# Kernel tuning notes

Hardware: AMD Instinct MI355X
Metric: run time of the kernel (lower is better)

## Reference

```python
import jax, jax.numpy as jnp
import numpy as np

N = 50000
E = 800000
R = 8
F_IN = 128
H = 128


def setup_inputs() -> dict:
    key = jax.random.key(0)
    ks = jax.random.split(key, 16)
    x = jax.random.normal(ks[0], (N, F_IN), dtype=jnp.float32)
    edge_index = jax.random.randint(ks[1], (2, E), 0, N, dtype=jnp.int64)
    edge_type = jax.random.randint(ks[2], (E,), 0, R, dtype=jnp.int64)
    s = 0.05
    params = {
        'W1': jax.random.normal(ks[3], (R, F_IN, H), jnp.float32) * s,
        'root1': jax.random.normal(ks[4], (F_IN, H), jnp.float32) * s,
        'b1': jnp.zeros((H,), jnp.float32),
        'W2': jax.random.normal(ks[5], (R, H, H), jnp.float32) * s,
        'root2': jax.random.normal(ks[6], (H, H), jnp.float32) * s,
        'b2': jnp.zeros((H,), jnp.float32),
        'W3': jax.random.normal(ks[7], (R, H, H), jnp.float32) * s,
        'root3': jax.random.normal(ks[8], (H, H), jnp.float32) * s,
        'b3': jnp.zeros((H,), jnp.float32),
        'fc_w': jax.random.normal(ks[9], (H, 1), jnp.float32) * s,
        'fc_b': jnp.zeros((1,), jnp.float32),
    }
    return dict(x=x, edge_index=edge_index, edge_type=edge_type, **params)


def _rgcn_conv(x, W, Wroot, b, src, dst, etype):
    # PyG RGCNConv with mean aggregation per (dst, relation):
    # out_i = x_i @ Wroot + b + sum_r mean_{j in N_r(i)} (x_j @ W_r)
    xw = jnp.einsum('nf,rfh->rnh', x, W)          # [R, N, H] per-relation transform
    m = xw[etype, src]                             # [E, H] gathered messages
    seg = dst * R + etype                          # composite (dst, rel) segment id
    deg = jax.ops.segment_sum(jnp.ones((m.shape[0],), x.dtype), seg, num_segments=N * R)
    norm = jnp.where(deg > 0, 1.0 / deg, 0.0)[seg]  # [E]
    agg = jax.ops.segment_sum(m * norm[:, None], dst, num_segments=N)  # [N, H]
    return agg + x @ Wroot + b


def reference(x, edge_index, edge_type, W1, root1, b1, W2, root2, b2, W3, root3, b3, fc_w, fc_b):
    src, dst = edge_index[0], edge_index[1]
    h = jax.nn.relu(_rgcn_conv(x, W1, root1, b1, src, dst, edge_type))
    h = jax.nn.relu(_rgcn_conv(h, W2, root2, b2, src, dst, edge_type))
    h = jax.nn.relu(_rgcn_conv(h, W3, root3, b3, src, dst, edge_type))
    out = h @ fc_w + fc_b                          # [N, 1]
    return out.reshape(-1)                         # [N]
```

## Files before the change

kernel.cpp:

```cpp
#include <hip/hip_runtime.h>

#define NN 50000
#define NPAD 50048
#define EE 800000
#define RR 8
#define NR (NN * RR)
#define KC 1152

typedef __attribute__((ext_vector_type(8))) short bf16x8;
typedef __attribute__((ext_vector_type(4))) float f32x4;

__device__ __forceinline__ unsigned short f2bf(float f) {
    unsigned u = __builtin_bit_cast(unsigned, f);
    u = (u + 0x7FFF + ((u >> 16) & 1)) >> 16;
    return (unsigned short)u;
}
__device__ __forceinline__ float bf2f(unsigned short s) {
    return __builtin_bit_cast(float, (unsigned)s << 16);
}

#define GLDS16(g, l) __builtin_amdgcn_global_load_lds( \
    (const __attribute__((address_space(1))) void*)(g), \
    (__attribute__((address_space(3))) void*)(l), 16, 0, 0)

__global__ void zero_i32(int* __restrict__ p, int n) {
    int i = blockIdx.x * blockDim.x + threadIdx.x;
    if (i < n) p[i] = 0;
}

__global__ void count_deg(const int* __restrict__ dst, const int* __restrict__ et,
                          int* __restrict__ degRel) {
    int e = blockIdx.x * blockDim.x + threadIdx.x;
    if (e < EE) atomicAdd(&degRel[dst[e] * RR + et[e]], 1);
}

__global__ void sum8(const int* __restrict__ degRel, int* __restrict__ degD) {
    int n = blockIdx.x * blockDim.x + threadIdx.x;
    if (n >= NN) return;
    int s = 0;
    #pragma unroll
    for (int r = 0; r < RR; ++r) s += degRel[n * RR + r];
    degD[n] = s;
}

__global__ __launch_bounds__(256) void scan1(const int* __restrict__ in, int* __restrict__ out,
                                             int* __restrict__ bsum, int n) {
    __shared__ int sh[256];
    int t = threadIdx.x;
    int base = blockIdx.x * 1024 + t * 4;
    int v[4]; int s = 0;
    #pragma unroll
    for (int i = 0; i < 4; ++i) { int idx = base + i; v[i] = (idx < n) ? in[idx] : 0; s += v[i]; }
    sh[t] = s; __syncthreads();
    for (int off = 1; off < 256; off <<= 1) {
        int x = (t >= off) ? sh[t - off] : 0; __syncthreads();
        if (t >= off) sh[t] += x; __syncthreads();
    }
    if (t == 255) bsum[blockIdx.x] = sh[255];
    int run = sh[t] - s;
    #pragma unroll
    for (int i = 0; i < 4; ++i) { int idx = base + i; if (idx < n) out[idx] = run; run += v[i]; }
}

__global__ __launch_bounds__(256) void scan2(int* __restrict__ bsum, int nb) {
    __shared__ int sh[256];
    int t = threadIdx.x; int carry = 0;
    for (int base = 0; base < nb; base += 256) {
        int idx = base + t;
        int v = (idx < nb) ? bsum[idx] : 0;
        sh[t] = v; __syncthreads();
        for (int off = 1; off < 256; off <<= 1) {
            int x = (t >= off) ? sh[t - off] : 0; __syncthreads();
            if (t >= off) sh[t] += x; __syncthreads();
        }
        int incl = sh[t];
        int total = sh[255];
        if (idx < nb) bsum[idx] = carry + incl - v;
        carry += total;
        __syncthreads();
    }
}

__global__ __launch_bounds__(256) void scan3(int* __restrict__ out, const int* __restrict__ bsum, int n) {
    int base = blockIdx.x * 1024 + threadIdx.x * 4;
    int add = bsum[blockIdx.x];
    #pragma unroll
    for (int i = 0; i < 4; ++i) { int idx = base + i; if (idx < n) out[idx] += add; }
}

__global__ void set_last(int* __restrict__ segD) {
    segD[NN] = EE;
}

__global__ void scatter2(const int* __restrict__ src, const int* __restrict__ dst,
                         const int* __restrict__ et, const int* __restrict__ segD,
                         const int* __restrict__ degRel, int* __restrict__ cursorD,
                         unsigned* __restrict__ rec) {
    int e = blockIdx.x * blockDim.x + threadIdx.x;
    if (e >= EE) return;
    int d_ = dst[e], r_ = et[e], s_ = src[e];
    int pos = segD[d_] + atomicAdd(&cursorD[d_], 1);
    int dg = degRel[d_ * RR + r_]; if (dg > 63) dg = 63;
    rec[pos] = ((unsigned)(s_ * KC + 128 + r_ * 128) << 6) | (unsigned)dg;
}

__global__ __launch_bounds__(256) void xcvt(const float* __restrict__ x,
                                            unsigned short* __restrict__ xbf) {
    size_t i = ((size_t)blockIdx.x * 256 + threadIdx.x) * 4;
    if (i >= (size_t)NPAD * 128) return;
    unsigned short o[4];
    if (i < (size_t)NN * 128) {
        float4 v = *reinterpret_cast<const float4*>(x + i);
        o[0] = f2bf(v.x); o[1] = f2bf(v.y); o[2] = f2bf(v.z); o[3] = f2bf(v.w);
    } else {
        o[0] = o[1] = o[2] = o[3] = 0;
    }
    unsigned lo = (unsigned)o[0] | ((unsigned)o[1] << 16);
    unsigned hi = (unsigned)o[2] | ((unsigned)o[3] << 16);
    *reinterpret_cast<uint2*>(xbf + i) = make_uint2(lo, hi);
}

__global__ void build_bt2(const float* __restrict__ W, const float* __restrict__ root,
                          unsigned short* __restrict__ Bt2) {
    int i = blockIdx.x * blockDim.x + threadIdx.x;
    if (i >= KC * 128) return;
    int col = i / 128, k = i % 128;
    float v;
    if (col < 128) v = root[k * 128 + col];
    else {
        int r = (col - 128) >> 7, cp = (col - 128) & 127;
        v = W[((size_t)r * 128 + k) * 128 + cp];
    }
    Bt2[i] = f2bf(v);
}

__global__ __launch_bounds__(256, 2) void gemm_y(
    const unsigned short* __restrict__ hin,
    const unsigned short* __restrict__ Bt2,
    unsigned short* __restrict__ y)
{
    __shared__ alignas(16) unsigned short Bs[2][128 * 128];
    const int tid = threadIdx.x;
    const int w = tid >> 6, lane = tid & 63;
    const int l15 = lane & 15, lhi = lane >> 4;
    const int row0 = blockIdx.x * 64;

    auto stage = [&](int b, int p) {
        #pragma unroll
        for (int i = 0; i < 8; ++i) {
            int q = i * 256 + tid;
            int col = q >> 4, c = q & 15;
            GLDS16(Bt2 + (size_t)(p * 128 + col) * 128 + ((c ^ (col & 7)) * 8), &Bs[b][q * 8]);
        }
    };

    const int gn = row0 + w * 16 + l15;
    const unsigned short* abase = hin + ((size_t)gn << 7) + lhi * 8;
    bf16x8 rf[4];
    rf[0] = *reinterpret_cast<const bf16x8*>(abase);
    rf[1] = *reinterpret_cast<const bf16x8*>(abase + 32);
    rf[2] = *reinterpret_cast<const bf16x8*>(abase + 64);
    rf[3] = *reinterpret_cast<const bf16x8*>(abase + 96);

    stage(0, 0);
    __syncthreads();
    for (int p = 0; p < 9; ++p) {
        const int b = p & 1;
        if (p < 8) stage(b ^ 1, p + 1);
        f32x4 acc[8];
        #pragma unroll
        for (int i = 0; i < 8; ++i) acc[i] = (f32x4)(0.f);
        #pragma unroll
        for (int s = 0; s < 4; ++s) {
            #pragma unroll
            for (int cg = 0; cg < 8; ++cg) {
                int col = cg * 16 + l15;
                int phys = (s * 4 + lhi) ^ (col & 7);
                bf16x8 bv = *reinterpret_cast<const bf16x8*>(&Bs[b][col * 128 + phys * 8]);
                acc[cg] = __builtin_amdgcn_mfma_f32_16x16x32_bf16(rf[s], bv, acc[cg], 0, 0, 0);
            }
        }
        #pragma unroll
        for (int cg = 0; cg < 8; ++cg) {
            int col = p * 128 + cg * 16 + l15;
            #pragma unroll
            for (int rg = 0; rg < 4; ++rg) {
                int grow = row0 + w * 16 + lhi * 4 + rg;
                y[(size_t)grow * KC + col] = f2bf(acc[cg][rg]);
            }
        }
        __syncthreads();
    }
}

template<bool FINAL>
__global__ __launch_bounds__(256) void agg3(
    const unsigned short* __restrict__ y,
    const unsigned* __restrict__ rec,
    const int* __restrict__ segD,
    const float* __restrict__ bias,
    unsigned short* __restrict__ hout,
    const float* __restrict__ fcw,
    const float* __restrict__ fcb,
    float* __restrict__ fout)
{
    const int w = threadIdx.x >> 6, lane = threadIdx.x & 63;
    const int n = blockIdx.x * 4 + w;
    if (n >= NPAD) return;
    const int fl = lane & 15, eg = lane >> 4;

    float fa[8];
    #pragma unroll
    for (int i = 0; i < 8; ++i) fa[i] = 0.f;

    if (n < NN) {
        const int s0 = segD[n], s1 = segD[n + 1];
        for (int base = s0; base < s1; base += 64) {
            const int ld = min(64, s1 - base);
            int idx = base + lane; if (idx > s1 - 1) idx = s1 - 1;
            const int rcL = (int)rec[idx];
            for (int t0 = 0; t0 < ld; t0 += 16) {
                uint4 L[4]; float nm[4];
                #pragma unroll
                for (int t = 0; t < 4; ++t) {
                    int j = t0 + t * 4 + eg;
                    int rcj = __shfl(rcL, j & 63);
                    bool on = (j < ld);
                    nm[t] = on ? __builtin_amdgcn_rcpf((float)(rcj & 63)) : 0.f;
                    unsigned off = ((unsigned)rcj) >> 6;
                    const unsigned short* p = y + (size_t)(on ? off : 0u) + fl * 8;
                    L[t] = *reinterpret_cast<const uint4*>(p);
                }
                #pragma unroll
                for (int t = 0; t < 4; ++t) {
                    fa[0] += nm[t] * bf2f((unsigned short)(L[t].x & 0xFFFF));
                    fa[1] += nm[t] * bf2f((unsigned short)(L[t].x >> 16));
                    fa[2] += nm[t] * bf2f((unsigned short)(L[t].y & 0xFFFF));
                    fa[3] += nm[t] * bf2f((unsigned short)(L[t].y >> 16));
                    fa[4] += nm[t] * bf2f((unsigned short)(L[t].z & 0xFFFF));
                    fa[5] += nm[t] * bf2f((unsigned short)(L[t].z >> 16));
                    fa[6] += nm[t] * bf2f((unsigned short)(L[t].w & 0xFFFF));
                    fa[7] += nm[t] * bf2f((unsigned short)(L[t].w >> 16));
                }
            }
        }
        #pragma unroll
        for (int i = 0; i < 8; ++i) {
            fa[i] += __shfl_xor(fa[i], 16);
            fa[i] += __shfl_xor(fa[i], 32);
        }
    }

    if (eg == 0) {
        if (n < NN) {
            const unsigned short* rp = y + (size_t)n * KC + fl * 8;
            uint4 rv = *reinterpret_cast<const uint4*>(rp);
            float4 b0 = *reinterpret_cast<const float4*>(bias + fl * 8);
            float4 b1 = *reinterpret_cast<const float4*>(bias + fl * 8 + 4);
            float r[8];
            r[0] = bf2f((unsigned short)(rv.x & 0xFFFF)); r[1] = bf2f((unsigned short)(rv.x >> 16));
            r[2] = bf2f((unsigned short)(rv.y & 0xFFFF)); r[3] = bf2f((unsigned short)(rv.y >> 16));
            r[4] = bf2f((unsigned short)(rv.z & 0xFFFF)); r[5] = bf2f((unsigned short)(rv.z >> 16));
            r[6] = bf2f((unsigned short)(rv.w & 0xFFFF)); r[7] = bf2f((unsigned short)(rv.w >> 16));
            float bb[8] = {b0.x, b0.y, b0.z, b0.w, b1.x, b1.y, b1.z, b1.w};
            float v[8];
            #pragma unroll
            for (int i = 0; i < 8; ++i) v[i] = fmaxf(fa[i] + r[i] + bb[i], 0.f);
            if constexpr (!FINAL) {
                uint4 pk;
                unsigned short o[8];
                #pragma unroll
                for (int i = 0; i < 8; ++i) o[i] = f2bf(v[i]);
                pk.x = (unsigned)o[0] | ((unsigned)o[1] << 16);
                pk.y = (unsigned)o[2] | ((unsigned)o[3] << 16);
                pk.z = (unsigned)o[4] | ((unsigned)o[5] << 16);
                pk.w = (unsigned)o[6] | ((unsigned)o[7] << 16);
                *reinterpret_cast<uint4*>(hout + (size_t)n * 128 + fl * 8) = pk;
            } else {
                float dp = 0.f;
                #pragma unroll
                for (int i = 0; i < 8; ++i) dp += bf2f(f2bf(v[i])) * fcw[fl * 8 + i];
                dp += __shfl_xor(dp, 1);
                dp += __shfl_xor(dp, 2);
                dp += __shfl_xor(dp, 4);
                dp += __shfl_xor(dp, 8);
                if (fl == 0) fout[n] = dp + fcb[0];
            }
        } else if constexpr (!FINAL) {
            *reinterpret_cast<uint4*>(hout + (size_t)n * 128 + fl * 8) = make_uint4(0, 0, 0, 0);
        }
    }
}

extern "C" void kernel_launch(void* const* d_in, const int* in_sizes, int n_in,
                              void* d_out, int out_size, void* d_ws, size_t ws_size,
                              hipStream_t stream) {
    const float* x     = (const float*)d_in[0];
    const int*   ei    = (const int*)d_in[1];
    const int*   etype = (const int*)d_in[2];
    const float* W[3]    = {(const float*)d_in[3], (const float*)d_in[6], (const float*)d_in[9]};
    const float* root[3] = {(const float*)d_in[4], (const float*)d_in[7], (const float*)d_in[10]};
    const float* bias[3] = {(const float*)d_in[5], (const float*)d_in[8], (const float*)d_in[11]};
    const float* fcw = (const float*)d_in[12];
    const float* fcb = (const float*)d_in[13];
    const int* src = ei;
    const int* dst = ei + EE;

    char* ws = (char*)d_ws;
    auto alloc = [&](size_t bytes) { char* p = ws; ws += (bytes + 255) & ~(size_t)255; return p; };
    int* degRel   = (int*)alloc(NR * sizeof(int));
    int* cursorD  = (int*)alloc(NN * sizeof(int));
    int* degD     = (int*)alloc(NN * sizeof(int));
    int* segD     = (int*)alloc((NN + 2) * sizeof(int));
    int* bsum     = (int*)alloc(512 * sizeof(int));
    unsigned* rec = (unsigned*)alloc((size_t)EE * sizeof(unsigned));
    unsigned short* Bt2g = (unsigned short*)alloc((size_t)3 * KC * 128 * sizeof(short));
    unsigned short* xbf  = (unsigned short*)alloc((size_t)NPAD * 128 * sizeof(short));
    unsigned short* h1   = (unsigned short*)alloc((size_t)NPAD * 128 * sizeof(short));
    unsigned short* h2   = (unsigned short*)alloc((size_t)NPAD * 128 * sizeof(short));
    unsigned short* yall = (unsigned short*)alloc((size_t)NPAD * KC * sizeof(short));

    zero_i32<<<(NR + NN + 255) / 256, 256, 0, stream>>>(degRel, NR + NN);
    count_deg<<<(EE + 255) / 256, 256, 0, stream>>>(dst, etype, degRel);
    sum8<<<(NN + 255) / 256, 256, 0, stream>>>(degRel, degD);
    const int nScanBlk = (NN + 1023) / 1024;
    scan1<<<nScanBlk, 256, 0, stream>>>(degD, segD, bsum, NN);
    scan2<<<1, 256, 0, stream>>>(bsum, nScanBlk);
    scan3<<<nScanBlk, 256, 0, stream>>>(segD, bsum, NN);
    set_last<<<1, 1, 0, stream>>>(segD);
    scatter2<<<(EE + 255) / 256, 256, 0, stream>>>(src, dst, etype, segD, degRel, cursorD, rec);

    xcvt<<<((NPAD * 128 / 4) + 255) / 256, 256, 0, stream>>>(x, xbf);
    const int btN = KC * 128;
    for (int l = 0; l < 3; ++l)
        build_bt2<<<(btN + 255) / 256, 256, 0, stream>>>(W[l], root[l], Bt2g + (size_t)l * btN);

    const int ggrid = NPAD / 64;
    const int aggGrid = NPAD / 4;
    const unsigned short* hin = xbf;
    unsigned short* houts[2] = {h1, h2};
    for (int l = 0; l < 3; ++l) {
        gemm_y<<<ggrid, 256, 0, stream>>>(hin, Bt2g + (size_t)l * btN, yall);
        if (l < 2) {
            agg3<false><<<aggGrid, 256, 0, stream>>>(yall, rec, segD, bias[l], houts[l],
                                                     nullptr, nullptr, nullptr);
            hin = houts[l];
        } else {
            agg3<true><<<aggGrid, 256, 0, stream>>>(yall, rec, segD, bias[l], nullptr,
                                                    fcw, fcb, (float*)d_out);
        }
    }
}
```

Before: 328.3 us.

## Pre-swizzle weights into MFMA fragment order and drop LDS staging in GEMM

Weights are laid out at build time in the exact per-lane MFMA fragment order, so gemm_y reads B fragments straight from global memory (L2-resident, shared by all blocks) rather than staging through double-buffered LDS with barriers. MFMA operands are swapped so each lane holds four consecutive output columns, which lets outputs be written as packed 8-byte stores instead of scattered 2-byte stores, and padded rows are skipped. This removes LDS traffic and __syncthreads, and frees occupancy, at the cost of more global/L2 loads per wave, since every wave fetches the full weight matrix itself.

Measured after the change: 428.3 us. 1.3x slower.

```diff
diff --git a/kernel.cpp b/kernel.cpp
--- a/kernel.cpp
+++ b/kernel.cpp
@@ -18,10 +18,6 @@
 __device__ __forceinline__ float bf2f(unsigned short s) {
     return __builtin_bit_cast(float, (unsigned)s << 16);
 }
-
-#define GLDS16(g, l) __builtin_amdgcn_global_load_lds( \
-    (const __attribute__((address_space(1))) void*)(g), \
-    (__attribute__((address_space(3))) void*)(l), 16, 0, 0)
 
 __global__ void zero_i32(int* __restrict__ p, int n) {
     int i = blockIdx.x * blockDim.x + threadIdx.x;
@@ -120,41 +116,33 @@
     *reinterpret_cast<uint2*>(xbf + i) = make_uint2(lo, hi);
 }
 
-__global__ void build_bt2(const float* __restrict__ W, const float* __restrict__ root,
-                          unsigned short* __restrict__ Bt2) {
+__global__ void build_bt3(const float* __restrict__ W, const float* __restrict__ root,
+                          unsigned short* __restrict__ Bf) {
     int i = blockIdx.x * blockDim.x + threadIdx.x;
-    if (i >= KC * 128) return;
-    int col = i / 128, k = i % 128;
+    if (i >= 9 * 8 * 4 * 64 * 8) return;
+    int e = i & 7, lane = (i >> 3) & 63, s = (i >> 9) & 3, cg = (i >> 11) & 7, p = i >> 14;
+    int col = p * 128 + cg * 16 + (lane & 15);
+    int k = (s * 4 + (lane >> 4)) * 8 + e;
     float v;
     if (col < 128) v = root[k * 128 + col];
     else {
         int r = (col - 128) >> 7, cp = (col - 128) & 127;
         v = W[((size_t)r * 128 + k) * 128 + cp];
     }
-    Bt2[i] = f2bf(v);
-}
-
-__global__ __launch_bounds__(256, 2) void gemm_y(
+    Bf[i] = f2bf(v);
+}
+
+__global__ __launch_bounds__(256) void gemm_y(
     const unsigned short* __restrict__ hin,
-    const unsigned short* __restrict__ Bt2,
+    const unsigned short* __restrict__ Bf,
     unsigned short* __restrict__ y)
 {
-    __shared__ alignas(16) unsigned short Bs[2][128 * 128];
     const int tid = threadIdx.x;
     const int w = tid >> 6, lane = tid & 63;
     const int l15 = lane & 15, lhi = lane >> 4;
     const int row0 = blockIdx.x * 64;
-
-    auto stage = [&](int b, int p) {
-        #pragma unroll
-        for (int i = 0; i < 8; ++i) {
-            int q = i * 256 + tid;
-            int col = q >> 4, c = q & 15;
-            GLDS16(Bt2 + (size_t)(p * 128 + col) * 128 + ((c ^ (col & 7)) * 8), &Bs[b][q * 8]);
-        }
-    };
-
     const int gn = row0 + w * 16 + l15;
+
     const unsigned short* abase = hin + ((size_t)gn << 7) + lhi * 8;
     bf16x8 rf[4];
     rf[0] = *reinterpret_cast<const bf16x8*>(abase);
@@ -162,11 +150,11 @@
     rf[2] = *reinterpret_cast<const bf16x8*>(abase + 64);
     rf[3] = *reinterpret_cast<const bf16x8*>(abase + 96);
 
-    stage(0, 0);
-    __syncthreads();
+    const unsigned short* bbase = Bf + lane * 8;
+    unsigned short* yrow = y + (size_t)gn * KC;
+    const bool wr = (gn < NN);
+
     for (int p = 0; p < 9; ++p) {
-        const int b = p & 1;
-        if (p < 8) stage(b ^ 1, p + 1);
         f32x4 acc[8];
         #pragma unroll
         for (int i = 0; i < 8; ++i) acc[i] = (f32x4)(0.f);
@@ -174,22 +162,20 @@
         for (int s = 0; s < 4; ++s) {
             #pragma unroll
             for (int cg = 0; cg < 8; ++cg) {
-                int col = cg * 16 + l15;
-                int phys = (s * 4 + lhi) ^ (col & 7);
-                bf16x8 bv = *reinterpret_cast<const bf16x8*>(&Bs[b][col * 128 + phys * 8]);
-                acc[cg] = __builtin_amdgcn_mfma_f32_16x16x32_bf16(rf[s], bv, acc[cg], 0, 0, 0);
+                bf16x8 bv = *reinterpret_cast<const bf16x8*>(
+                    bbase + (size_t)(((p * 8 + cg) * 4 + s) * 64) * 8);
+                acc[cg] = __builtin_amdgcn_mfma_f32_16x16x32_bf16(bv, rf[s], acc[cg], 0, 0, 0);
             }
         }
-        #pragma unroll
-        for (int cg = 0; cg < 8; ++cg) {
-            int col = p * 128 + cg * 16 + l15;
+        if (wr) {
             #pragma unroll
-            for (int rg = 0; rg < 4; ++rg) {
-                int grow = row0 + w * 16 + lhi * 4 + rg;
-                y[(size_t)grow * KC + col] = f2bf(acc[cg][rg]);
+            for (int cg = 0; cg < 8; ++cg) {
+                uint2 pk;
+                pk.x = (unsigned)f2bf(acc[cg][0]) | ((unsigned)f2bf(acc[cg][1]) << 16);
+                pk.y = (unsigned)f2bf(acc[cg][2]) | ((unsigned)f2bf(acc[cg][3]) << 16);
+                *reinterpret_cast<uint2*>(yrow + p * 128 + cg * 16 + lhi * 4) = pk;
             }
         }
-        __syncthreads();
     }
 }
 
@@ -314,7 +300,7 @@
     int* segD     = (int*)alloc((NN + 2) * sizeof(int));
     int* bsum     = (int*)alloc(512 * sizeof(int));
     unsigned* rec = (unsigned*)alloc((size_t)EE * sizeof(unsigned));
-    unsigned short* Bt2g = (unsigned short*)alloc((size_t)3 * KC * 128 * sizeof(short));
+    unsigned short* Bfg  = (unsigned short*)alloc((size_t)3 * KC * 128 * sizeof(short));
     unsigned short* xbf  = (unsigned short*)alloc((size_t)NPAD * 128 * sizeof(short));
     unsigned short* h1   = (unsigned short*)alloc((size_t)NPAD * 128 * sizeof(short));
     unsigned short* h2   = (unsigned short*)alloc((size_t)NPAD * 128 * sizeof(short));
@@ -333,14 +319,14 @@
     xcvt<<<((NPAD * 128 / 4) + 255) / 256, 256, 0, stream>>>(x, xbf);
     const int btN = KC * 128;
     for (int l = 0; l < 3; ++l)
-        build_bt2<<<(btN + 255) / 256, 256, 0, stream>>>(W[l], root[l], Bt2g + (size_t)l * btN);
+        build_bt3<<<(btN + 255) / 256, 256, 0, stream>>>(W[l], root[l], Bfg + (size_t)l * btN);
 
     const int ggrid = NPAD / 64;
     const int aggGrid = NPAD / 4;
     const unsigned short* hin = xbf;
     unsigned short* houts[2] = {h1, h2};
     for (int l = 0; l < 3; ++l) {
-        gemm_y<<<ggrid, 256, 0, stream>>>(hin, Bt2g + (size_t)l * btN, yall);
+        gemm_y<<<ggrid, 256, 0, stream>>>(hin, Bfg + (size_t)l * btN, yall);
         if (l < 2) {
             agg3<false><<<aggGrid, 256, 0, stream>>>(yall, rec, segD, bias[l], houts[l],
                                                      nullptr, nullptr, nullptr);
```
